# Kernel optimization log

Hardware: AMD Instinct MI355X
Metric: run time of the kernel (lower is better)

## Reference

```python
import jax, jax.numpy as jnp
import numpy as np

EPS_SUM = 1e-8
EPS_FILL = 1e-4
NORM_THRESH = 0.1
MASK_THRESH = 0.1


def _shift1(x):
    # conv2d with 1x3 filter [1,1,0], padding (0,1): out[i] = x[i-1] + x[i]
    return x + jnp.pad(x, ((0, 0), (0, 0), (0, 0), (1, 0)))[..., :-1]


def _shift2(x):
    # conv2d with 1x3 filter [0,1,1], padding (0,1): out[i] = x[i] + x[i+1]
    return x + jnp.pad(x, ((0, 0), (0, 0), (0, 0), (0, 1)))[..., 1:]


def _fill(disp, vm, shift_fn, n_steps):
    # Hole filling: each step propagates valid disparity one pixel; after W
    # steps the data-dependent while-loop of the original has converged
    # (further steps are identity), so a fixed-length scan is equivalent.
    def step(carry, _):
        d, m = carry
        m1 = shift_fn(m)
        nm = (m1 > 0).astype(d.dtype)
        d = d * m + shift_fn(d) / (m1 + EPS_FILL) * (nm - m)
        return (d, nm), None
    (disp, vm), _ = jax.lax.scan(step, (disp, vm), None, length=n_steps)
    return disp, vm


def regress_disp(att, valid_mask):
    # att: [B,H,W,W], valid_mask: [B,1,H,W]
    b, h, w, _ = att.shape
    idx = jnp.arange(w, dtype=att.dtype)
    disp_ini = idx[None, None, None, :] - jnp.sum(att * idx, axis=-1).reshape(b, 1, h, w)
    disp = disp_ini * valid_mask
    disp, vm = _fill(disp, valid_mask, _shift1, w)  # left-to-right pass
    disp, vm = _fill(disp, vm, _shift2, w)          # right-to-left pass
    return disp_ini * valid_mask + disp * (1.0 - valid_mask)


def masked_exp_norm(cost, lower):
    # tril/triu-masked exp normalization (non-standard attention)
    tri = jnp.tril if lower else jnp.triu
    c = tri(cost)
    c = jnp.exp(c - jnp.max(c, axis=-1, keepdims=True))
    c = tri(c)
    return c / (jnp.sum(c, axis=-1, keepdims=True) + EPS_SUM)


def gen_pos_shift(w, dtype):
    p = jnp.linspace(0.0, 2.0, w).astype(dtype)
    pos = jnp.maximum(p[:, None] - p[None, :], 0.0)  # pos_l - pos_r, clipped
    return pos[None, None]  # [1,1,W,W]


def gen_raw_disp(att, pos_shift):
    hi = jnp.argmax(att, axis=-1)
    rr = jnp.stack([hi - 1, hi, hi + 1], axis=-1) + 1  # indices into padded axis
    att_pad = jnp.pad(att, ((0, 0), (0, 0), (0, 0), (1, 1)))
    aw = jnp.take_along_axis(att_pad, rr, axis=-1)
    norm = jnp.sum(aw, axis=-1, keepdims=True)
    norm = jnp.where(norm < NORM_THRESH, 1.0, norm)
    aw = aw / norm
    pos_pad = jnp.broadcast_to(jnp.pad(pos_shift, ((0, 0), (0, 0), (0, 0), (1, 1))), att_pad.shape)
    pr = jnp.take_along_axis(pos_pad, rr, axis=-1)
    return jnp.sum(aw * pr, axis=-1)  # [B,H,W]


def setup_inputs() -> dict:
    key = jax.random.key(0)
    k1, k2 = jax.random.split(key)
    B, H, W = 1, 64, 512
    cost1 = jax.random.normal(k1, (B, H, W, W), dtype=jnp.float32)
    cost2 = jax.random.normal(k2, (B, H, W, W), dtype=jnp.float32)
    return {"cost1": cost1, "cost2": cost2}


def reference(cost1, cost2):
    b, h, w, _ = cost1.shape
    att_r2l = masked_exp_norm(cost2, lower=True)   # right-to-left attention
    att_l2r = masked_exp_norm(cost1, lower=False)  # left-to-right attention
    vm_left = (jnp.sum(att_l2r, axis=-2) > MASK_THRESH).astype(cost1.dtype).reshape(b, 1, h, w)
    vm_right = (jnp.sum(att_r2l, axis=-2) > MASK_THRESH).astype(cost1.dtype).reshape(b, 1, h, w)
    disp_r2l = regress_disp(att_r2l, vm_left)   # [B,1,H,W]
    disp_l2r = regress_disp(att_l2r, vm_right)  # [B,1,H,W]
    pos = gen_pos_shift(w, cost1.dtype)
    raw_l2r = gen_raw_disp(att_r2l, pos)                               # [B,H,W]
    raw_r2l = gen_raw_disp(att_l2r, jnp.swapaxes(pos, -1, -2))         # [B,H,W]
    return jnp.concatenate([disp_r2l, disp_l2r, raw_l2r[:, None], raw_r2l[:, None]], axis=1)
```

## Files before the change

### kernel.cpp

```cpp
#include <hip/hip_runtime.h>
#include <float.h>

#define H 64
#define W 512
#define SPLIT 4

template<bool LOWER>
__global__ __launch_bounds__(512) void attn_stats(
    const float* __restrict__ cost,
    float* __restrict__ disp_ini,
    float* __restrict__ colsum,
    float* __restrict__ raw)
{
  __shared__ float scol[W];
  const int tid  = threadIdx.x;
  const int lane = tid & 63;
  const int wid  = tid >> 6;
  const int h    = blockIdx.x / SPLIT;
  const int s    = blockIdx.x % SPLIT;
  scol[tid] = 0.f;
  __syncthreads();

  float cacc[8] = {0,0,0,0,0,0,0,0};
  const float pscale = 2.0f / 511.0f;
  const float* hb = cost + (size_t)h * W * W;

  int jmap[8];
  #pragma unroll
  for (int k = 0; k < 8; k++)
    jmap[k] = (k < 4) ? (lane * 4 + k) : (256 + lane * 4 + (k - 4));

  for (int t = wid; t < W / SPLIT; t += 8) {
    const int i = s * (W / SPLIT) + t;
    const float* rp = hb + (size_t)i * W;
    const float4 va = ((const float4*)rp)[lane];
    const float4 vb = ((const float4*)rp)[64 + lane];
    float c[8] = {va.x, va.y, va.z, va.w, vb.x, vb.y, vb.z, vb.w};

    bool vld[8];
    float mx = -FLT_MAX;
    #pragma unroll
    for (int k = 0; k < 8; k++) {
      vld[k] = LOWER ? (jmap[k] <= i) : (jmap[k] >= i);
      if (vld[k] && c[k] > mx) mx = c[k];
    }
    #pragma unroll
    for (int off = 32; off; off >>= 1) mx = fmaxf(mx, __shfl_xor(mx, off));
    if (LOWER ? (i < W - 1) : (i > 0)) mx = fmaxf(mx, 0.f);

    float e[8];
    float ssum = 0.f, wsum = 0.f, bv = -1.f;
    int bi = 0;
    #pragma unroll
    for (int k = 0; k < 8; k++) {
      e[k] = vld[k] ? __expf(c[k] - mx) : 0.f;
      ssum += e[k];
      wsum += e[k] * (float)jmap[k];
      if (e[k] > bv) { bv = e[k]; bi = jmap[k]; }
    }
    #pragma unroll
    for (int off = 32; off; off >>= 1) {
      ssum += __shfl_xor(ssum, off);
      wsum += __shfl_xor(wsum, off);
      const float ov = __shfl_xor(bv, off);
      const int   oi = __shfl_xor(bi, off);
      if (ov > bv || (ov == bv && oi < bi)) { bv = ov; bi = oi; }
    }
    const float inv = 1.0f / (ssum + 1e-8f);
    const int hi = bi;

    float t0 = 0.f, t1 = 0.f;
    #pragma unroll
    for (int k = 0; k < 8; k++) {
      const float att = e[k] * inv;
      cacc[k] += att;
      if (jmap[k] >= hi - 1 && jmap[k] <= hi + 1) {
        const float pr = LOWER ? fmaxf((float)(i - jmap[k]) * pscale, 0.f)
                               : fmaxf((float)(jmap[k] - i) * pscale, 0.f);
        t0 += att;
        t1 += att * pr;
      }
    }
    #pragma unroll
    for (int off = 32; off; off >>= 1) {
      t0 += __shfl_xor(t0, off);
      t1 += __shfl_xor(t1, off);
    }
    if (lane == 0) {
      disp_ini[h * W + i] = (float)i - wsum * inv;
      raw[h * W + i]      = t1 / (t0 < 0.1f ? 1.0f : t0);
    }
  }

  #pragma unroll
  for (int k = 0; k < 8; k++) atomicAdd(&scol[jmap[k]], cacc[k]);
  __syncthreads();
  atomicAdd(&colsum[h * W + tid], scol[tid]);
}

__global__ __launch_bounds__(64) void fill_rows(
    const float* __restrict__ dispA, const float* __restrict__ csA,
    const float* __restrict__ dispB, const float* __restrict__ csB,
    float* __restrict__ out)
{
  __shared__ float xrow[W];
  const int pair = blockIdx.x >> 6;
  const int h    = blockIdx.x & 63;
  const float* dsp = (pair ? dispB : dispA) + h * W;
  const float* cs  = (pair ? csB  : csA ) + h * W;
  float* o = out + pair * (H * W) + h * W;
  const int lane = threadIdx.x;
  const int j0 = lane * 8;

  float x[8];
  bool m[8];
  int incl[8];
  int run = -1, fv = W;
  #pragma unroll
  for (int k = 0; k < 8; k++) {
    x[k] = dsp[j0 + k];
    m[k] = cs[j0 + k] > 0.1f;
    xrow[j0 + k] = x[k];
    if (m[k]) { run = j0 + k; if (fv == W) fv = j0 + k; }
    incl[k] = run;
  }
  int v = run;
  #pragma unroll
  for (int off = 1; off < 64; off <<= 1) {
    const int tv = __shfl_up(v, off);
    if (lane >= off) v = max(v, tv);
  }
  int excl = __shfl_up(v, 1);
  if (lane == 0) excl = -1;
  int p0 = fv;
  #pragma unroll
  for (int off = 32; off; off >>= 1) p0 = min(p0, __shfl_xor(p0, off));
  __syncthreads();

  const float C2 = -1.4426229e-4f;
  #pragma unroll
  for (int k = 0; k < 8; k++) {
    const int jj = j0 + k;
    float ov;
    if (m[k]) {
      ov = x[k];
    } else {
      const int p = max(excl, incl[k]);
      if (p >= 0)        ov = xrow[p]  * exp2f(C2 * (float)(jj - p));
      else if (p0 < W)   ov = xrow[p0] * exp2f(C2 * (float)(p0 - jj));
      else               ov = 0.f;
    }
    o[jj] = ov;
  }
}

extern "C" void kernel_launch(void* const* d_in, const int* in_sizes, int n_in,
                              void* d_out, int out_size, void* d_ws, size_t ws_size,
                              hipStream_t stream) {
  const float* cost1 = (const float*)d_in[0];
  const float* cost2 = (const float*)d_in[1];
  float* out = (float*)d_out;
  float* w = (float*)d_ws;
  float* disp_r2l_ini = w;
  float* disp_l2r_ini = w + 32768;
  float* cs_l2r       = w + 65536;
  float* cs_r2l       = w + 98304;

  hipMemsetAsync(cs_l2r, 0, 2 * (size_t)H * W * sizeof(float), stream);

  attn_stats<true ><<<H * SPLIT, 512, 0, stream>>>(cost2, disp_r2l_ini, cs_r2l,
                                                   out + 2 * H * W);
  attn_stats<false><<<H * SPLIT, 512, 0, stream>>>(cost1, disp_l2r_ini, cs_l2r,
                                                   out + 3 * H * W);
  fill_rows<<<2 * H, 64, 0, stream>>>(disp_r2l_ini, cs_l2r,
                                      disp_l2r_ini, cs_r2l, out);
}
```

Measured before the change: 197.1 us.

## Merge both attention-stat kernels into one launch and compute argmax from raw costs

Fuses the lower and upper attention-statistics kernels into a single launch that interleaves blocks for both cost tensors, and doubles SPLIT so 1024 blocks cover the GPU instead of two launches of 256. The argmax is now taken from raw masked costs during the max reduction, so the 3-tap sums are gathered with two lane shuffles instead of a full wave reduction over normalized values. This removes one launch gap and a reduction tree per row, but adds more column-sum atomics and a runtime branch on the triangle direction.

```diff
diff --git a/kernel.cpp b/kernel.cpp
--- a/kernel.cpp
+++ b/kernel.cpp
@@ -3,21 +3,29 @@
 
 #define H 64
 #define W 512
-#define SPLIT 4
+#define SPLIT 8
 
-template<bool LOWER>
-__global__ __launch_bounds__(512) void attn_stats(
-    const float* __restrict__ cost,
-    float* __restrict__ disp_ini,
-    float* __restrict__ colsum,
-    float* __restrict__ raw)
+__global__ __launch_bounds__(512) void attn_stats_all(
+    const float* __restrict__ cost1, const float* __restrict__ cost2,
+    float* __restrict__ disp_r2l, float* __restrict__ disp_l2r,
+    float* __restrict__ cs_r2l,  float* __restrict__ cs_l2r,
+    float* __restrict__ out)
 {
   __shared__ float scol[W];
   const int tid  = threadIdx.x;
   const int lane = tid & 63;
   const int wid  = tid >> 6;
-  const int h    = blockIdx.x / SPLIT;
-  const int s    = blockIdx.x % SPLIT;
+  const int gid  = blockIdx.x;
+  const bool lower = (gid & 1) == 0;
+  const int rest = gid >> 1;
+  const int h    = rest / SPLIT;
+  const int s    = rest % SPLIT;
+
+  const float* cost = lower ? cost2 : cost1;
+  float* disp = lower ? disp_r2l : disp_l2r;
+  float* csum = lower ? cs_r2l  : cs_l2r;
+  float* raw  = out + (lower ? 2 : 3) * (H * W);
+
   scol[tid] = 0.f;
   __syncthreads();
 
@@ -38,64 +46,64 @@
     float c[8] = {va.x, va.y, va.z, va.w, vb.x, vb.y, vb.z, vb.w};
 
     bool vld[8];
-    float mx = -FLT_MAX;
+    float mxv = -FLT_MAX;
+    int   bj  = W;
     #pragma unroll
     for (int k = 0; k < 8; k++) {
-      vld[k] = LOWER ? (jmap[k] <= i) : (jmap[k] >= i);
-      if (vld[k] && c[k] > mx) mx = c[k];
+      vld[k] = lower ? (jmap[k] <= i) : (jmap[k] >= i);
+      if (vld[k] && c[k] > mxv) { mxv = c[k]; bj = jmap[k]; }
     }
     #pragma unroll
-    for (int off = 32; off; off >>= 1) mx = fmaxf(mx, __shfl_xor(mx, off));
-    if (LOWER ? (i < W - 1) : (i > 0)) mx = fmaxf(mx, 0.f);
+    for (int off = 32; off; off >>= 1) {
+      const float ov = __shfl_xor(mxv, off);
+      const int   oj = __shfl_xor(bj, off);
+      if (ov > mxv || (ov == mxv && oj < bj)) { mxv = ov; bj = oj; }
+    }
+    const int hi = bj;
+    float mx = mxv;
+    if (lower ? (i < W - 1) : (i > 0)) mx = fmaxf(mx, 0.f);
 
     float e[8];
-    float ssum = 0.f, wsum = 0.f, bv = -1.f;
-    int bi = 0;
+    float ssum = 0.f, wsum = 0.f, s0 = 0.f, s1 = 0.f;
     #pragma unroll
     for (int k = 0; k < 8; k++) {
       e[k] = vld[k] ? __expf(c[k] - mx) : 0.f;
       ssum += e[k];
       wsum += e[k] * (float)jmap[k];
-      if (e[k] > bv) { bv = e[k]; bi = jmap[k]; }
+      if (jmap[k] >= hi - 1 && jmap[k] <= hi + 1) {
+        const float pr = fmaxf((float)(lower ? (i - jmap[k]) : (jmap[k] - i)) * pscale, 0.f);
+        s0 += e[k];
+        s1 += e[k] * pr;
+      }
     }
     #pragma unroll
     for (int off = 32; off; off >>= 1) {
       ssum += __shfl_xor(ssum, off);
       wsum += __shfl_xor(wsum, off);
-      const float ov = __shfl_xor(bv, off);
-      const int   oi = __shfl_xor(bi, off);
-      if (ov > bv || (ov == bv && oi < bi)) { bv = ov; bi = oi; }
     }
     const float inv = 1.0f / (ssum + 1e-8f);
-    const int hi = bi;
 
-    float t0 = 0.f, t1 = 0.f;
+    const int jlo = hi > 0 ? hi - 1 : 0;
+    const int jh2 = hi < W - 1 ? hi + 1 : W - 1;
+    const int l1 = (jlo & 255) >> 2;
+    const int l2 = (jh2 & 255) >> 2;
+    float t0 = __shfl(s0, l1), t1 = __shfl(s1, l1);
+    if (l2 != l1) { t0 += __shfl(s0, l2); t1 += __shfl(s1, l2); }
+
     #pragma unroll
-    for (int k = 0; k < 8; k++) {
-      const float att = e[k] * inv;
-      cacc[k] += att;
-      if (jmap[k] >= hi - 1 && jmap[k] <= hi + 1) {
-        const float pr = LOWER ? fmaxf((float)(i - jmap[k]) * pscale, 0.f)
-                               : fmaxf((float)(jmap[k] - i) * pscale, 0.f);
-        t0 += att;
-        t1 += att * pr;
-      }
-    }
-    #pragma unroll
-    for (int off = 32; off; off >>= 1) {
-      t0 += __shfl_xor(t0, off);
-      t1 += __shfl_xor(t1, off);
-    }
+    for (int k = 0; k < 8; k++) cacc[k] += e[k] * inv;
+
     if (lane == 0) {
-      disp_ini[h * W + i] = (float)i - wsum * inv;
-      raw[h * W + i]      = t1 / (t0 < 0.1f ? 1.0f : t0);
+      disp[h * W + i] = (float)i - wsum * inv;
+      const float n0 = t0 * inv;
+      raw[h * W + i]  = (t1 * inv) / (n0 < 0.1f ? 1.0f : n0);
     }
   }
 
   #pragma unroll
   for (int k = 0; k < 8; k++) atomicAdd(&scol[jmap[k]], cacc[k]);
   __syncthreads();
-  atomicAdd(&colsum[h * W + tid], scol[tid]);
+  atomicAdd(&csum[h * W + tid], scol[tid]);
 }
 
 __global__ __launch_bounds__(64) void fill_rows(
@@ -168,10 +176,9 @@
 
   hipMemsetAsync(cs_l2r, 0, 2 * (size_t)H * W * sizeof(float), stream);
 
-  attn_stats<true ><<<H * SPLIT, 512, 0, stream>>>(cost2, disp_r2l_ini, cs_r2l,
-                                                   out + 2 * H * W);
-  attn_stats<false><<<H * SPLIT, 512, 0, stream>>>(cost1, disp_l2r_ini, cs_l2r,
-                                                   out + 3 * H * W);
+  attn_stats_all<<<2 * H * SPLIT, 512, 0, stream>>>(
+      cost1, cost2, disp_r2l_ini, disp_l2r_ini, cs_r2l, cs_l2r, out);
+
   fill_rows<<<2 * H, 64, 0, stream>>>(disp_r2l_ini, cs_l2r,
                                       disp_l2r_ini, cs_r2l, out);
 }
```

After: 170.8 us. 1.15x faster.
